# Performance work log

Measured on AMD Instinct MI355X. Metric: run time of the kernel, lower is better.

The kernel has to match this reference:

```python
import jax, jax.numpy as jnp
import numpy as np

SUBSTEPS = 2  # fixed RK4 substeps per observation interval (replaces adaptive Tsit5)


def setup_inputs() -> dict:
    key = jax.random.key(0)
    k1, k2, k3, k4, k5 = jax.random.split(key, 5)
    n, d, c, T = 20000, 64, 8, 8
    m, nnz = 5000, 320000
    return {
        "y0": jax.random.normal(k1, (n, d), dtype=jnp.float32),
        "ts": jnp.arange(T, dtype=jnp.float32),
        "controls": jax.random.normal(k2, (T, n, c), dtype=jnp.float32),
        "W": 0.05 * jax.random.normal(k3, (d, d * c), dtype=jnp.float32),
        "b": jnp.zeros((d * c,), dtype=jnp.float32),
        "node_idx": jax.random.randint(k4, (nnz,), 0, n, dtype=jnp.int32),
        "edge_idx": jax.random.randint(k5, (nnz,), 0, m, dtype=jnp.int32),
        "num_edges": m,
    }


def reference(y0, ts, controls, W, b, node_idx, edge_idx, num_edges):
    n, d = y0.shape
    c = controls.shape[-1]
    m = int(num_edges)

    ones = jnp.ones(node_idx.shape[0], dtype=y0.dtype)
    edge_deg = jnp.maximum(jax.ops.segment_sum(ones, edge_idx, num_segments=m), 1.0)
    node_deg = jnp.maximum(jax.ops.segment_sum(ones, node_idx, num_segments=n), 1.0)

    def conv(y):  # HGNN-style two-hop mean aggregation, then linear (n,d)->(n,d*c)
        e = jax.ops.segment_sum(y[node_idx], edge_idx, num_segments=m) / edge_deg[:, None]
        agg = jax.ops.segment_sum(e[edge_idx], node_idx, num_segments=n) / node_deg[:, None]
        return agg @ W + b

    # backward Hermite spline knot derivatives (diffrax backward_hermite_coefficients)
    dt = (ts[1:] - ts[:-1])[:, None, None]            # (T-1,1,1)
    diffs = (controls[1:] - controls[:-1]) / dt        # (T-1,n,c)
    derivs = jnp.concatenate([diffs[:1], diffs], 0)    # (T,n,c)

    def control_deriv(t, seg):  # dX/dt on interval via cubic Hermite basis derivatives
        h = seg["t1"] - seg["t0"]
        s = (t - seg["t0"]) / h
        return (((6 * s * s - 6 * s) / h) * seg["x0"]
                + (3 * s * s - 4 * s + 1) * seg["d0"]
                + ((-6 * s * s + 6 * s) / h) * seg["x1"]
                + (3 * s * s - 2 * s) * seg["d1"])

    def drift(t, y, seg):  # f(y) reshaped (n,d,c), contracted with dX/dt (n,c)
        raw = jnp.tanh(conv(y))
        mat = raw.reshape(n, d, c)
        return jnp.einsum('ndc,nc->nd', mat, control_deriv(t, seg))

    def interval_step(y, seg):
        h = (seg["t1"] - seg["t0"]) / SUBSTEPS
        for k in range(SUBSTEPS):
            t = seg["t0"] + k * h
            k1 = drift(t, y, seg)
            k2 = drift(t + 0.5 * h, y + 0.5 * h * k1, seg)
            k3 = drift(t + 0.5 * h, y + 0.5 * h * k2, seg)
            k4 = drift(t + h, y + h * k3, seg)
            y = y + (h / 6.0) * (k1 + 2 * k2 + 2 * k3 + k4)
        return y, y

    segs = {"t0": ts[:-1], "t1": ts[1:],
            "x0": controls[:-1], "x1": controls[1:],
            "d0": derivs[:-1], "d1": derivs[1:]}
    _, ys_tail = jax.lax.scan(interval_step, y0, segs)
    return jnp.concatenate([y0[None], ys_tail], axis=0)  # (T,n,d)
```

## Files before the change

kernel.cpp:

```cpp
#include <hip/hip_runtime.h>


typedef __attribute__((ext_vector_type(8))) short bfrag8;
typedef __attribute__((ext_vector_type(4))) float f32x4;

__device__ __forceinline__ float bf2f(ushort u) {
  union { uint i; float f; } v; v.i = (uint)u << 16; return v.f;
}
__device__ __forceinline__ ushort f2bf(float f) {
  union { uint i; float f; } v; v.f = f;
  uint r = v.i + 0x7fff + ((v.i >> 16) & 1);
  return (ushort)(r >> 16);
}
__device__ __forceinline__ uint pack2(float lo, float hi) {
  return ((uint)f2bf(hi) << 16) | (uint)f2bf(lo);
}

__global__ __launch_bounds__(256) void k_count(const int* __restrict__ node_idx,
                                               const int* __restrict__ edge_idx,
                                               int* __restrict__ cnt_e,
                                               int* __restrict__ cnt_n, int nnz) {
  int j = blockIdx.x * 256 + threadIdx.x;
  if (j < nnz) {
    atomicAdd(&cnt_e[edge_idx[j]], 1);
    atomicAdd(&cnt_n[node_idx[j]], 1);
  }
}

__global__ __launch_bounds__(1024) void k_scan(const int* __restrict__ cnt,
                                               int* __restrict__ off,
                                               int* __restrict__ cur, int len) {
  __shared__ int sd[1024];
  __shared__ int s_run;
  if (threadIdx.x == 0) s_run = 0;
  __syncthreads();
  for (int base = 0; base < len; base += 1024) {
    int i = base + threadIdx.x;
    int v = (i < len) ? cnt[i] : 0;
    sd[threadIdx.x] = v;
    __syncthreads();
    for (int ofs = 1; ofs < 1024; ofs <<= 1) {
      int tv = (threadIdx.x >= ofs) ? sd[threadIdx.x - ofs] : 0;
      __syncthreads();
      sd[threadIdx.x] += tv;
      __syncthreads();
    }
    int run = s_run;
    if (i < len) {
      int excl = run + sd[threadIdx.x] - v;
      off[i] = excl;
      cur[i] = excl;
    }
    __syncthreads();
    if (threadIdx.x == 1023) s_run = run + sd[1023];
    __syncthreads();
  }
  if (threadIdx.x == 0) off[len] = s_run;
}

__global__ __launch_bounds__(256) void k_fill(const int* __restrict__ node_idx,
                                              const int* __restrict__ edge_idx,
                                              int* __restrict__ cur_e,
                                              int* __restrict__ cur_n,
                                              int* __restrict__ csr_e,
                                              int* __restrict__ csr_n, int nnz) {
  int j = blockIdx.x * 256 + threadIdx.x;
  if (j < nnz) {
    int v = node_idx[j], e = edge_idx[j];
    int pe = atomicAdd(&cur_e[e], 1);
    csr_e[pe] = v;
    int pn = atomicAdd(&cur_n[v], 1);
    csr_n[pn] = e;
  }
}

__global__ __launch_bounds__(256) void k_invdeg(const int* __restrict__ cnt_e,
                                                const int* __restrict__ cnt_n,
                                                float* __restrict__ inv_e,
                                                float* __restrict__ inv_n,
                                                int m, int n) {
  int i = blockIdx.x * 256 + threadIdx.x;
  if (i < m) inv_e[i] = 1.f / (float)max(cnt_e[i], 1);
  if (i < n) inv_n[i] = 1.f / (float)max(cnt_n[i], 1);
}

__global__ __launch_bounds__(256) void k_prep(const float* __restrict__ W,
                                              const float* __restrict__ y0,
                                              ushort* __restrict__ Wt,
                                              ushort* __restrict__ y0bf,
                                              int nW, int nY) {
  int stride = gridDim.x * 256;
  for (int i = blockIdx.x * 256 + threadIdx.x; i < nY; i += stride)
    y0bf[i] = f2bf(y0[i]);
  for (int i = blockIdx.x * 256 + threadIdx.x; i < nW; i += stride) {
    int k = i >> 9, c = i & 511;
    Wt[c * 64 + k] = f2bf(W[i]);
  }
}

__device__ __forceinline__ void seg_gather(const uint* __restrict__ src,
                                           const int* __restrict__ csr,
                                           int p, int pe, int cp,
                                           float& A0, float& A1) {
  float a0 = 0.f, a1 = 0.f, b0 = 0.f, b1 = 0.f;
  for (; p + 6 < pe; p += 8) {
    int r0 = csr[p], r1 = csr[p + 2], r2 = csr[p + 4], r3 = csr[p + 6];
    uint v0 = src[(size_t)r0 * 32 + cp];
    uint v1 = src[(size_t)r1 * 32 + cp];
    uint v2 = src[(size_t)r2 * 32 + cp];
    uint v3 = src[(size_t)r3 * 32 + cp];
    a0 += bf2f((ushort)(v0 & 0xffff)) + bf2f((ushort)(v2 & 0xffff));
    a1 += bf2f((ushort)(v0 >> 16)) + bf2f((ushort)(v2 >> 16));
    b0 += bf2f((ushort)(v1 & 0xffff)) + bf2f((ushort)(v3 & 0xffff));
    b1 += bf2f((ushort)(v1 >> 16)) + bf2f((ushort)(v3 >> 16));
  }
  if (p + 2 < pe) {
    int r0 = csr[p], r1 = csr[p + 2];
    uint v0 = src[(size_t)r0 * 32 + cp];
    uint v1 = src[(size_t)r1 * 32 + cp];
    a0 += bf2f((ushort)(v0 & 0xffff));
    a1 += bf2f((ushort)(v0 >> 16));
    b0 += bf2f((ushort)(v1 & 0xffff));
    b1 += bf2f((ushort)(v1 >> 16));
    p += 4;
  }
  if (p < pe) {
    uint v0 = src[(size_t)csr[p] * 32 + cp];
    a0 += bf2f((ushort)(v0 & 0xffff));
    a1 += bf2f((ushort)(v0 >> 16));
  }
  A0 = a0 + b0;
  A1 = a1 + b1;
}

__global__ __launch_bounds__(256) void k_seg_mean_bf(const uint* __restrict__ src,
                                                     const int* __restrict__ off,
                                                     const int* __restrict__ csr,
                                                     const float* __restrict__ invdeg,
                                                     uint* __restrict__ dst,
                                                     int nseg) {
  int gid = blockIdx.x * 256 + threadIdx.x;
  int seg = gid >> 6;
  if (seg >= nseg) return;
  int lane = gid & 63;
  int half = lane >> 5;
  int cp = lane & 31;
  float a0, a1;
  seg_gather(src, csr, off[seg] + half, off[seg + 1], cp, a0, a1);
  a0 += __shfl_xor(a0, 32);
  a1 += __shfl_xor(a1, 32);
  if (half == 0) {
    float s = invdeg[seg];
    dst[(size_t)seg * 32 + cp] = pack2(a0 * s, a1 * s);
  }
}

__global__ __launch_bounds__(256) void k_drift_f(
    const uint* __restrict__ e_bf,
    const int* __restrict__ off_n, const int* __restrict__ csr_n,
    const float* __restrict__ invdeg_n,
    const ushort* __restrict__ Wt, const float* __restrict__ bvec,
    const float* __restrict__ controls, const float* __restrict__ ts,
    const float* __restrict__ y_base, float* __restrict__ acc_out,
    uint* __restrict__ ybf,
    int t, int stage, int substep, int n) {
  __shared__ uint aggs[16][36];
  __shared__ float Us[16][8];
  __shared__ float kvs[16][68];

  const int tid = threadIdx.x;
  const int w = tid >> 6;
  const int lane = tid & 63;
  const int half = lane >> 5;
  const int cp = lane & 31;
  const int nodebase = blockIdx.x * 16;

  float t0v = ts[t], t1v = ts[t + 1];
  float h = t1v - t0v;
  float hs = 0.5f * h;
  float soff = (stage == 1) ? 0.f : (stage == 4) ? 1.f : 0.5f;
  float s = ((float)substep + soff) * 0.5f;
  float s2 = s * s;
  float cx0 = (6.f * s2 - 6.f * s) / h;
  float cd0 = 3.f * s2 - 4.f * s + 1.f;
  float cx1 = (-6.f * s2 + 6.f * s) / h;
  float cd1 = 3.f * s2 - 2.f * s;
  float a_m1, a_0, a_p1;
  if (t == 0) {
    a_m1 = 0.f;
    a_0 = cx0 - cd1 / h - cd0 / h;
    a_p1 = cx1 + cd1 / h + cd0 / h;
  } else {
    float hm = t0v - ts[t - 1];
    a_m1 = -cd0 / hm;
    a_0 = cx0 - cd1 / h + cd0 / hm;
    a_p1 = cx1 + cd1 / h;
  }
  int tm1 = (t > 0) ? t - 1 : 0;
  float wk = ((stage == 2 || stage == 3) ? 2.f : 1.f) * hs * (1.f / 6.f);
  float cst = (stage == 3) ? hs : 0.5f * hs;

  const int nl4 = tid >> 4;
  const int f0 = (tid & 15) * 4;
  const size_t o4 = (size_t)(nodebase + nl4) * 64 + f0;
  float4 ya = *reinterpret_cast<const float4*>(y_base + o4);
  float4 pa = ya;
  if (stage != 1) pa = *reinterpret_cast<const float4*>(acc_out + o4);

  if (tid < 128) {
    int nl = tid >> 3, ci = tid & 7;
    size_t bi = (size_t)(nodebase + nl) * 8 + ci;
    float c0 = controls[(size_t)t * n * 8 + bi];
    float cp1 = controls[(size_t)(t + 1) * n * 8 + bi];
    float cm1 = controls[(size_t)tm1 * n * 8 + bi];
    Us[nl][ci] = a_m1 * cm1 + a_0 * c0 + a_p1 * cp1;
  }

  #pragma unroll 1
  for (int rd = 0; rd < 4; ++rd) {
    int nl = rd * 4 + w;
    int gnode = nodebase + nl;
    float a0, a1;
    seg_gather(e_bf, csr_n, off_n[gnode] + half, off_n[gnode + 1], cp, a0, a1);
    a0 += __shfl_xor(a0, 32);
    a1 += __shfl_xor(a1, 32);
    if (half == 0) {
      float sc = invdeg_n[gnode];
      aggs[nl][cp] = pack2(a0 * sc, a1 * sc);
    }
  }
  __syncthreads();

  int arow = lane & 15;
  int kof4 = (lane >> 4) * 4;
  bfrag8 af0 = *reinterpret_cast<const bfrag8*>(&aggs[arow][kof4]);
  bfrag8 af1 = *reinterpret_cast<const bfrag8*>(&aggs[arow][kof4 + 16]);
  int ci = lane & 7, g8 = (lane >> 3) & 1;
  int rbase = (lane >> 4) * 4;
  float u_r[4];
  #pragma unroll
  for (int r = 0; r < 4; ++r) u_r[r] = Us[rbase + r][ci];

  #pragma unroll 2
  for (int ct = 0; ct < 8; ++ct) {
    int col = w * 128 + ct * 16 + (lane & 15);
    const ushort* wb = Wt + (size_t)col * 64 + (lane >> 4) * 8;
    bfrag8 b0 = *reinterpret_cast<const bfrag8*>(wb);
    bfrag8 b1 = *reinterpret_cast<const bfrag8*>(wb + 32);
    f32x4 acc = (f32x4){0.f, 0.f, 0.f, 0.f};
    acc = __builtin_amdgcn_mfma_f32_16x16x32_bf16(af0, b0, acc, 0, 0, 0);
    acc = __builtin_amdgcn_mfma_f32_16x16x32_bf16(af1, b1, acc, 0, 0, 0);
    float bb = bvec[col];
    int ddl = (w << 4) + ct * 2 + g8;
    #pragma unroll
    for (int r = 0; r < 4; ++r) {
      float x = acc[r] + bb;
      float th = 1.f - 2.f / (__expf(2.f * x) + 1.f);
      float v = th * u_r[r];
      v += __shfl_xor(v, 1);
      v += __shfl_xor(v, 2);
      v += __shfl_xor(v, 4);
      if (ci == 0) kvs[rbase + r][ddl] = v;
    }
  }
  __syncthreads();

  {
    float4 kv = *reinterpret_cast<float4*>(&kvs[nl4][f0]);
    float4 na;
    na.x = pa.x + wk * kv.x; na.y = pa.y + wk * kv.y;
    na.z = pa.z + wk * kv.z; na.w = pa.w + wk * kv.w;
    *reinterpret_cast<float4*>(acc_out + o4) = na;
    float4 sa;
    if (stage < 4) {
      sa.x = ya.x + cst * kv.x; sa.y = ya.y + cst * kv.y;
      sa.z = ya.z + cst * kv.z; sa.w = ya.w + cst * kv.w;
    } else sa = na;
    uint2 pk;
    pk.x = pack2(sa.x, sa.y);
    pk.y = pack2(sa.z, sa.w);
    *reinterpret_cast<uint2*>(ybf + ((size_t)(nodebase + nl4) * 32 + f0 / 2)) = pk;
  }
}

extern "C" void kernel_launch(void* const* d_in, const int* in_sizes, int n_in,
                              void* d_out, int out_size, void* d_ws, size_t ws_size,
                              hipStream_t stream) {
  const float* y0 = (const float*)d_in[0];
  const float* ts = (const float*)d_in[1];
  const float* controls = (const float*)d_in[2];
  const float* W = (const float*)d_in[3];
  const float* bvec = (const float*)d_in[4];
  const int* node_idx = (const int*)d_in[5];
  const int* edge_idx = (const int*)d_in[6];

  const int d = 64;
  const int n = in_sizes[0] / d;
  const int T = in_sizes[1];
  const int nnz = in_sizes[5];
  const int m = 5000;

  char* p = (char*)d_ws;
  auto carve = [&](size_t bytes) {
    char* r = p;
    p += (bytes + 255) & ~(size_t)255;
    return r;
  };
  int* cnt_e = (int*)carve((size_t)m * 4);
  int* cnt_n = (int*)carve((size_t)n * 4);
  int* off_e = (int*)carve((size_t)(m + 1) * 4);
  int* cur_e = (int*)carve((size_t)m * 4);
  int* off_n = (int*)carve((size_t)(n + 1) * 4);
  int* cur_n = (int*)carve((size_t)n * 4);
  int* csr_e = (int*)carve((size_t)nnz * 4);
  int* csr_n = (int*)carve((size_t)nnz * 4);
  float* invdeg_e = (float*)carve((size_t)m * 4);
  float* invdeg_n = (float*)carve((size_t)n * 4);
  ushort* Wt = (ushort*)carve((size_t)512 * 64 * 2);
  ushort* ybf = (ushort*)carve((size_t)n * d * 2);
  ushort* e_bf = (ushort*)carve((size_t)m * d * 2);
  float* y_mid = (float*)carve((size_t)n * d * 4);

  hipMemsetAsync(cnt_e, 0, (size_t)m * 4, stream);
  hipMemsetAsync(cnt_n, 0, (size_t)n * 4, stream);

  k_prep<<<1250, 256, 0, stream>>>(W, y0, Wt, ybf, 64 * 512, n * d);
  k_count<<<(nnz + 255) / 256, 256, 0, stream>>>(node_idx, edge_idx, cnt_e, cnt_n, nnz);
  k_scan<<<1, 1024, 0, stream>>>(cnt_e, off_e, cur_e, m);
  k_scan<<<1, 1024, 0, stream>>>(cnt_n, off_n, cur_n, n);
  k_fill<<<(nnz + 255) / 256, 256, 0, stream>>>(node_idx, edge_idx, cur_e, cur_n, csr_e, csr_n, nnz);
  int mx = (m > n) ? m : n;
  k_invdeg<<<(mx + 255) / 256, 256, 0, stream>>>(cnt_e, cnt_n, invdeg_e, invdeg_n, m, n);

  float* out = (float*)d_out;
  hipMemcpyAsync(out, y0, (size_t)n * d * sizeof(float), hipMemcpyDeviceToDevice, stream);

  const int gE = (m * 64 + 255) / 256;
  const int gT = n / 16;

  for (int t = 0; t < T - 1; ++t) {
    float* yout_i = out + (size_t)(t + 1) * n * d;
    for (int sub = 0; sub < 2; ++sub) {
      const float* yb = (sub == 0) ? (out + (size_t)t * n * d) : y_mid;
      float* accp = (sub == 0) ? y_mid : yout_i;
      for (int st = 1; st <= 4; ++st) {
        k_seg_mean_bf<<<gE, 256, 0, stream>>>((const uint*)ybf, off_e, csr_e,
                                              invdeg_e, (uint*)e_bf, m);
        k_drift_f<<<gT, 256, 0, stream>>>((const uint*)e_bf, off_n, csr_n,
                                          invdeg_n, Wt, bvec, controls, ts,
                                          yb, accp, (uint*)ybf, t, st, sub, n);
      }
    }
  }
}
```

Before: 2.116 ms.

## Widen drift blocks to one wave per node, fuse setup kernels, deepen gather unroll

```diff
diff --git a/kernel.cpp b/kernel.cpp
--- a/kernel.cpp
+++ b/kernel.cpp
@@ -19,17 +19,35 @@
 __global__ __launch_bounds__(256) void k_count(const int* __restrict__ node_idx,
                                                const int* __restrict__ edge_idx,
                                                int* __restrict__ cnt_e,
-                                               int* __restrict__ cnt_n, int nnz) {
+                                               int* __restrict__ cnt_n, int nnz,
+                                               const float* __restrict__ W,
+                                               const float* __restrict__ y0,
+                                               ushort* __restrict__ Wt,
+                                               ushort* __restrict__ y0bf,
+                                               int nW, int nY) {
   int j = blockIdx.x * 256 + threadIdx.x;
   if (j < nnz) {
     atomicAdd(&cnt_e[edge_idx[j]], 1);
     atomicAdd(&cnt_n[node_idx[j]], 1);
   }
-}
-
-__global__ __launch_bounds__(1024) void k_scan(const int* __restrict__ cnt,
-                                               int* __restrict__ off,
-                                               int* __restrict__ cur, int len) {
+  int stride = gridDim.x * 256;
+  for (int i = j; i < nY; i += stride) y0bf[i] = f2bf(y0[i]);
+  for (int i = j; i < nW; i += stride) {
+    int k = i >> 9, c = i & 511;
+    Wt[c * 64 + k] = f2bf(W[i]);
+  }
+}
+
+__global__ __launch_bounds__(1024) void k_scan2(const int* __restrict__ cnt_e,
+                                                int* __restrict__ off_e,
+                                                int* __restrict__ cur_e, int m,
+                                                const int* __restrict__ cnt_n,
+                                                int* __restrict__ off_n,
+                                                int* __restrict__ cur_n, int n) {
+  const int* cnt = (blockIdx.x == 0) ? cnt_e : cnt_n;
+  int* off = (blockIdx.x == 0) ? off_e : off_n;
+  int* cur = (blockIdx.x == 0) ? cur_e : cur_n;
+  int len = (blockIdx.x == 0) ? m : n;
   __shared__ int sd[1024];
   __shared__ int s_run;
   if (threadIdx.x == 0) s_run = 0;
@@ -63,7 +81,12 @@
                                               int* __restrict__ cur_e,
                                               int* __restrict__ cur_n,
                                               int* __restrict__ csr_e,
-                                              int* __restrict__ csr_n, int nnz) {
+                                              int* __restrict__ csr_n, int nnz,
+                                              const int* __restrict__ cnt_e,
+                                              const int* __restrict__ cnt_n,
+                                              float* __restrict__ inv_e,
+                                              float* __restrict__ inv_n,
+                                              int m, int n) {
   int j = blockIdx.x * 256 + threadIdx.x;
   if (j < nnz) {
     int v = node_idx[j], e = edge_idx[j];
@@ -72,30 +95,8 @@
     int pn = atomicAdd(&cur_n[v], 1);
     csr_n[pn] = e;
   }
-}
-
-__global__ __launch_bounds__(256) void k_invdeg(const int* __restrict__ cnt_e,
-                                                const int* __restrict__ cnt_n,
-                                                float* __restrict__ inv_e,
-                                                float* __restrict__ inv_n,
-                                                int m, int n) {
-  int i = blockIdx.x * 256 + threadIdx.x;
-  if (i < m) inv_e[i] = 1.f / (float)max(cnt_e[i], 1);
-  if (i < n) inv_n[i] = 1.f / (float)max(cnt_n[i], 1);
-}
-
-__global__ __launch_bounds__(256) void k_prep(const float* __restrict__ W,
-                                              const float* __restrict__ y0,
-                                              ushort* __restrict__ Wt,
-                                              ushort* __restrict__ y0bf,
-                                              int nW, int nY) {
-  int stride = gridDim.x * 256;
-  for (int i = blockIdx.x * 256 + threadIdx.x; i < nY; i += stride)
-    y0bf[i] = f2bf(y0[i]);
-  for (int i = blockIdx.x * 256 + threadIdx.x; i < nW; i += stride) {
-    int k = i >> 9, c = i & 511;
-    Wt[c * 64 + k] = f2bf(W[i]);
-  }
+  if (j < m) inv_e[j] = 1.f / (float)max(cnt_e[j], 1);
+  if (j < n) inv_n[j] = 1.f / (float)max(cnt_n[j], 1);
 }
 
 __device__ __forceinline__ void seg_gather(const uint* __restrict__ src,
@@ -103,7 +104,27 @@
                                            int p, int pe, int cp,
                                            float& A0, float& A1) {
   float a0 = 0.f, a1 = 0.f, b0 = 0.f, b1 = 0.f;
-  for (; p + 6 < pe; p += 8) {
+  for (; p + 14 < pe; p += 16) {
+    int r0 = csr[p],      r1 = csr[p + 2],  r2 = csr[p + 4],  r3 = csr[p + 6];
+    int r4 = csr[p + 8],  r5 = csr[p + 10], r6 = csr[p + 12], r7 = csr[p + 14];
+    uint v0 = src[(size_t)r0 * 32 + cp];
+    uint v1 = src[(size_t)r1 * 32 + cp];
+    uint v2 = src[(size_t)r2 * 32 + cp];
+    uint v3 = src[(size_t)r3 * 32 + cp];
+    uint v4 = src[(size_t)r4 * 32 + cp];
+    uint v5 = src[(size_t)r5 * 32 + cp];
+    uint v6 = src[(size_t)r6 * 32 + cp];
+    uint v7 = src[(size_t)r7 * 32 + cp];
+    a0 += bf2f((ushort)(v0 & 0xffff)) + bf2f((ushort)(v2 & 0xffff))
+        + bf2f((ushort)(v4 & 0xffff)) + bf2f((ushort)(v6 & 0xffff));
+    a1 += bf2f((ushort)(v0 >> 16)) + bf2f((ushort)(v2 >> 16))
+        + bf2f((ushort)(v4 >> 16)) + bf2f((ushort)(v6 >> 16));
+    b0 += bf2f((ushort)(v1 & 0xffff)) + bf2f((ushort)(v3 & 0xffff))
+        + bf2f((ushort)(v5 & 0xffff)) + bf2f((ushort)(v7 & 0xffff));
+    b1 += bf2f((ushort)(v1 >> 16)) + bf2f((ushort)(v3 >> 16))
+        + bf2f((ushort)(v5 >> 16)) + bf2f((ushort)(v7 >> 16));
+  }
+  if (p + 6 < pe) {
     int r0 = csr[p], r1 = csr[p + 2], r2 = csr[p + 4], r3 = csr[p + 6];
     uint v0 = src[(size_t)r0 * 32 + cp];
     uint v1 = src[(size_t)r1 * 32 + cp];
@@ -113,6 +134,7 @@
     a1 += bf2f((ushort)(v0 >> 16)) + bf2f((ushort)(v2 >> 16));
     b0 += bf2f((ushort)(v1 & 0xffff)) + bf2f((ushort)(v3 & 0xffff));
     b1 += bf2f((ushort)(v1 >> 16)) + bf2f((ushort)(v3 >> 16));
+    p += 8;
   }
   if (p + 2 < pe) {
     int r0 = csr[p], r1 = csr[p + 2];
@@ -145,17 +167,16 @@
   int lane = gid & 63;
   int half = lane >> 5;
   int cp = lane & 31;
+  float sc = invdeg[seg];
   float a0, a1;
   seg_gather(src, csr, off[seg] + half, off[seg + 1], cp, a0, a1);
   a0 += __shfl_xor(a0, 32);
   a1 += __shfl_xor(a1, 32);
-  if (half == 0) {
-    float s = invdeg[seg];
-    dst[(size_t)seg * 32 + cp] = pack2(a0 * s, a1 * s);
-  }
-}
-
-__global__ __launch_bounds__(256) void k_drift_f(
+  if (half == 0)
+    dst[(size_t)seg * 32 + cp] = pack2(a0 * sc, a1 * sc);
+}
+
+__global__ __launch_bounds__(1024, 8) void k_drift_f(
     const uint* __restrict__ e_bf,
     const int* __restrict__ off_n, const int* __restrict__ csr_n,
     const float* __restrict__ invdeg_n,
@@ -200,13 +221,6 @@
   float wk = ((stage == 2 || stage == 3) ? 2.f : 1.f) * hs * (1.f / 6.f);
   float cst = (stage == 3) ? hs : 0.5f * hs;
 
-  const int nl4 = tid >> 4;
-  const int f0 = (tid & 15) * 4;
-  const size_t o4 = (size_t)(nodebase + nl4) * 64 + f0;
-  float4 ya = *reinterpret_cast<const float4*>(y_base + o4);
-  float4 pa = ya;
-  if (stage != 1) pa = *reinterpret_cast<const float4*>(acc_out + o4);
-
   if (tid < 128) {
     int nl = tid >> 3, ci = tid & 7;
     size_t bi = (size_t)(nodebase + nl) * 8 + ci;
@@ -216,18 +230,14 @@
     Us[nl][ci] = a_m1 * cm1 + a_0 * c0 + a_p1 * cp1;
   }
 
-  #pragma unroll 1
-  for (int rd = 0; rd < 4; ++rd) {
-    int nl = rd * 4 + w;
-    int gnode = nodebase + nl;
+  {
+    int gnode = nodebase + w;
+    float sc = invdeg_n[gnode];
     float a0, a1;
     seg_gather(e_bf, csr_n, off_n[gnode] + half, off_n[gnode + 1], cp, a0, a1);
     a0 += __shfl_xor(a0, 32);
     a1 += __shfl_xor(a1, 32);
-    if (half == 0) {
-      float sc = invdeg_n[gnode];
-      aggs[nl][cp] = pack2(a0 * sc, a1 * sc);
-    }
+    if (half == 0) aggs[w][cp] = pack2(a0 * sc, a1 * sc);
   }
   __syncthreads();
 
@@ -241,9 +251,9 @@
   #pragma unroll
   for (int r = 0; r < 4; ++r) u_r[r] = Us[rbase + r][ci];
 
-  #pragma unroll 2
-  for (int ct = 0; ct < 8; ++ct) {
-    int col = w * 128 + ct * 16 + (lane & 15);
+  #pragma unroll
+  for (int ctl = 0; ctl < 2; ++ctl) {
+    int col = w * 32 + ctl * 16 + (lane & 15);
     const ushort* wb = Wt + (size_t)col * 64 + (lane >> 4) * 8;
     bfrag8 b0 = *reinterpret_cast<const bfrag8*>(wb);
     bfrag8 b1 = *reinterpret_cast<const bfrag8*>(wb + 32);
@@ -251,7 +261,7 @@
     acc = __builtin_amdgcn_mfma_f32_16x16x32_bf16(af0, b0, acc, 0, 0, 0);
     acc = __builtin_amdgcn_mfma_f32_16x16x32_bf16(af1, b1, acc, 0, 0, 0);
     float bb = bvec[col];
-    int ddl = (w << 4) + ct * 2 + g8;
+    int ddl = w * 4 + ctl * 2 + g8;
     #pragma unroll
     for (int r = 0; r < 4; ++r) {
       float x = acc[r] + bb;
@@ -265,8 +275,14 @@
   }
   __syncthreads();
 
-  {
+  if (tid < 256) {
+    int nl4 = tid >> 4;
+    int f0 = (tid & 15) * 4;
+    size_t o4 = (size_t)(nodebase + nl4) * 64 + f0;
     float4 kv = *reinterpret_cast<float4*>(&kvs[nl4][f0]);
+    float4 ya = *reinterpret_cast<const float4*>(y_base + o4);
+    float4 pa = ya;
+    if (stage != 1) pa = *reinterpret_cast<const float4*>(acc_out + o4);
     float4 na;
     na.x = pa.x + wk * kv.x; na.y = pa.y + wk * kv.y;
     na.z = pa.z + wk * kv.z; na.w = pa.w + wk * kv.w;
@@ -324,13 +340,12 @@
   hipMemsetAsync(cnt_e, 0, (size_t)m * 4, stream);
   hipMemsetAsync(cnt_n, 0, (size_t)n * 4, stream);
 
-  k_prep<<<1250, 256, 0, stream>>>(W, y0, Wt, ybf, 64 * 512, n * d);
-  k_count<<<(nnz + 255) / 256, 256, 0, stream>>>(node_idx, edge_idx, cnt_e, cnt_n, nnz);
-  k_scan<<<1, 1024, 0, stream>>>(cnt_e, off_e, cur_e, m);
-  k_scan<<<1, 1024, 0, stream>>>(cnt_n, off_n, cur_n, n);
-  k_fill<<<(nnz + 255) / 256, 256, 0, stream>>>(node_idx, edge_idx, cur_e, cur_n, csr_e, csr_n, nnz);
-  int mx = (m > n) ? m : n;
-  k_invdeg<<<(mx + 255) / 256, 256, 0, stream>>>(cnt_e, cnt_n, invdeg_e, invdeg_n, m, n);
+  k_count<<<(nnz + 255) / 256, 256, 0, stream>>>(node_idx, edge_idx, cnt_e, cnt_n,
+                                                 nnz, W, y0, Wt, ybf, 64 * 512, n * d);
+  k_scan2<<<2, 1024, 0, stream>>>(cnt_e, off_e, cur_e, m, cnt_n, off_n, cur_n, n);
+  k_fill<<<(nnz + 255) / 256, 256, 0, stream>>>(node_idx, edge_idx, cur_e, cur_n,
+                                                csr_e, csr_n, nnz, cnt_e, cnt_n,
+                                                invdeg_e, invdeg_n, m, n);
 
   float* out = (float*)d_out;
   hipMemcpyAsync(out, y0, (size_t)n * d * sizeof(float), hipMemcpyDeviceToDevice, stream);
@@ -346,9 +361,9 @@
       for (int st = 1; st <= 4; ++st) {
         k_seg_mean_bf<<<gE, 256, 0, stream>>>((const uint*)ybf, off_e, csr_e,
                                               invdeg_e, (uint*)e_bf, m);
-        k_drift_f<<<gT, 256, 0, stream>>>((const uint*)e_bf, off_n, csr_n,
-                                          invdeg_n, Wt, bvec, controls, ts,
-                                          yb, accp, (uint*)ybf, t, st, sub, n);
+        k_drift_f<<<gT, 1024, 0, stream>>>((const uint*)e_bf, off_n, csr_n,
+                                           invdeg_n, Wt, bvec, controls, ts,
+                                           yb, accp, (uint*)ybf, t, st, sub, n);
       }
     }
   }
```

Result: faster. 1.913 ms (-9.6%).
